# Kernel optimization log

Measured on AMD Instinct MI355X. Metric: run time of the kernel, lower is better.

## Reference

```python
import jax, jax.numpy as jnp
import numpy as np

U = 128            # channel (mode) size after split_mode
NUM_OUT_SEG = 16   # output segments


def setup_inputs() -> dict:
    key = jax.random.key(0)
    ks = jax.random.split(key, 16)
    B = 16384          # batch (num nodes)
    NUM_X0 = 10        # weight table rows (e.g. chemical elements)
    C = 300            # num_couplings (x0 segments)
    S = 32             # num_in_segments (x1 segments)
    P1, P2, P3 = 32, 64, 96  # paths per correlation degree 1,2,3
    inp = {
        'x0': jax.random.normal(ks[0], (NUM_X0, C * U), dtype=jnp.float32),
        'i0': jax.random.randint(ks[1], (B,), 0, NUM_X0),
        'x1': jax.random.normal(ks[2], (B, S * U), dtype=jnp.float32),
        'idx1': jax.random.randint(ks[3], (P1, 1), 0, S),
        'w1': jax.random.randint(ks[4], (P1,), 0, C),
        'o1': jax.random.randint(ks[5], (P1,), 0, NUM_OUT_SEG),
        'c1': jax.random.normal(ks[6], (P1,), dtype=jnp.float32),
        'idx2': jax.random.randint(ks[7], (P2, 2), 0, S),
        'w2': jax.random.randint(ks[8], (P2,), 0, C),
        'o2': jax.random.randint(ks[9], (P2,), 0, NUM_OUT_SEG),
        'c2': jax.random.normal(ks[10], (P2,), dtype=jnp.float32),
        'idx3': jax.random.randint(ks[11], (P3, 3), 0, S),
        'w3': jax.random.randint(ks[12], (P3,), 0, C),
        'o3': jax.random.randint(ks[13], (P3,), 0, NUM_OUT_SEG),
        'c3': jax.random.normal(ks[14], (P3,), dtype=jnp.float32),
    }
    return inp


def _symmetric_contraction(x0, i0, x1, paths):
    # x0: (num_x0, C*U) weight table, i0: (B,) gather index, x1: (B, S*U)
    B = x1.shape[0]
    g0 = x0.reshape(x0.shape[0], -1, U)[i0]   # (B, C, U) indexed gather
    x1r = x1.reshape(B, -1, U)                # (B, S, U)
    out = jnp.zeros((NUM_OUT_SEG, B, U), dtype=x1.dtype)
    for idx, w, o, c in paths:
        # path product: coeff * x0[i0][w_p] * prod_k x1[idx_{p,k}]
        t = g0[:, w] * c[None, :, None]       # (B, P, U)
        for k in range(idx.shape[1]):          # degree <= 3 (static)
            t = t * x1r[:, idx[:, k]]
        # scatter-add over output segments
        out = out + jax.ops.segment_sum(t.transpose(1, 0, 2), o,
                                        num_segments=NUM_OUT_SEG)
    return out.transpose(1, 0, 2).reshape(B, NUM_OUT_SEG * U)


def reference(x0, i0, x1, idx1, w1, o1, c1, idx2, w2, o2, c2,
              idx3, w3, o3, c3):
    paths = ((idx1, w1, o1, c1), (idx2, w2, o2, c2), (idx3, w3, o3, c3))
    return _symmetric_contraction(x0, i0, x1, paths)
```

## Files before the change

### kernel.cpp

```cpp
#include <hip/hip_runtime.h>
#include <hip/hip_bf16.h>

#define U_DIM 128
#define NUM_OUT_SEG 16
#define C_DIM 300
#define S_DIM 32
#define NUM_X0 10
#define P1 32
#define P2 64
#define P3 96
#define P_TOT (P1 + P2 + P3)

typedef float vfloat4 __attribute__((ext_vector_type(4)));

__global__ void prep_kernel(const int* __restrict__ idx1, const int* __restrict__ w1,
                            const int* __restrict__ o1, const float* __restrict__ c1,
                            const int* __restrict__ idx2, const int* __restrict__ w2,
                            const int* __restrict__ o2, const float* __restrict__ c2,
                            const int* __restrict__ idx3, const int* __restrict__ w3,
                            const int* __restrict__ o3, const float* __restrict__ c3,
                            int* __restrict__ soff, int2* __restrict__ meta) {
    __shared__ int cnt[48];
    __shared__ int off[49];
    __shared__ int cur[48];
    const int t = threadIdx.x;
    if (t < 48) cnt[t] = 0;
    __syncthreads();

    int key = -1, packed = 0;
    float c = 0.f;
    if (t < P_TOT) {
        int deg, o, w, a0 = 0, a1 = 0, a2 = 0;
        if (t < P1) {
            int p = t;
            deg = 1; w = w1[p]; o = o1[p]; c = c1[p];
            a0 = idx1[p];
        } else if (t < P1 + P2) {
            int p = t - P1;
            deg = 2; w = w2[p]; o = o2[p]; c = c2[p];
            a0 = idx2[2 * p]; a1 = idx2[2 * p + 1];
        } else {
            int p = t - P1 - P2;
            deg = 3; w = w3[p]; o = o3[p]; c = c3[p];
            a0 = idx3[3 * p]; a1 = idx3[3 * p + 1]; a2 = idx3[3 * p + 2];
        }
        key = o * 3 + (deg - 1);
        packed = w | (a0 << 9) | (a1 << 14) | (a2 << 19);
        atomicAdd(&cnt[key], 1);
    }
    __syncthreads();
    if (t == 0) {
        int a = 0;
        for (int k = 0; k < 48; ++k) { off[k] = a; a += cnt[k]; }
        off[48] = a;
    }
    __syncthreads();
    if (t < 49) soff[t] = off[t];
    if (t < 48) cur[t] = off[t];
    __syncthreads();
    if (t < P_TOT) {
        int r = atomicAdd(&cur[key], 1);
        meta[r] = make_int2(packed, __float_as_int(c));
    }
}

__global__ __launch_bounds__(1024, 8) void contract_kernel(
    const float* __restrict__ x0, const int* __restrict__ i0,
    const float* __restrict__ x1, const int* __restrict__ soff,
    const int2* __restrict__ gmeta, float* __restrict__ out) {
    __shared__ vfloat4 x1s[2 * S_DIM * 32];
    __shared__ int2 smeta[P_TOT];

    const int tid = threadIdx.x;
    const int wave = tid >> 6;
    const int lane = tid & 63;
    const int h = lane >> 5;
    const int ch = lane & 31;
    const long b0 = (long)blockIdx.x * 2;

    const vfloat4* x1p = (const vfloat4*)(x1 + b0 * (S_DIM * U_DIM));
    x1s[tid] = x1p[tid];
    x1s[tid + 1024] = x1p[tid + 1024];
    if (tid < P_TOT) smeta[tid] = gmeta[tid];

    const int elem = i0[b0 + h];
    const vfloat4* gseg = (const vfloat4*)x0 + (long)elem * (C_DIM * 32) + ch;
    const vfloat4* myx1 = x1s + h * (S_DIM * 32) + ch;

    int p = soff[wave * 3];
    const int e1 = soff[wave * 3 + 1];
    const int e2 = soff[wave * 3 + 2];
    const int e3 = soff[wave * 3 + 3];
    __syncthreads();

    vfloat4 acc = (vfloat4)(0.f);

#pragma unroll 2
    for (; p < e1; ++p) {
        int2 m = smeta[p];
        float cc = __int_as_float(m.y);
        vfloat4 g = gseg[(m.x & 0x1FF) * 32];
        vfloat4 xa = myx1[((m.x >> 9) & 31) * 32];
        acc += (cc * g) * xa;
    }
#pragma unroll 2
    for (; p < e2; ++p) {
        int2 m = smeta[p];
        float cc = __int_as_float(m.y);
        vfloat4 g = gseg[(m.x & 0x1FF) * 32];
        vfloat4 xa = myx1[((m.x >> 9) & 31) * 32];
        vfloat4 xb = myx1[((m.x >> 14) & 31) * 32];
        acc += (cc * g) * (xa * xb);
    }
#pragma unroll 2
    for (; p < e3; ++p) {
        int2 m = smeta[p];
        float cc = __int_as_float(m.y);
        vfloat4 g = gseg[(m.x & 0x1FF) * 32];
        vfloat4 xa = myx1[((m.x >> 9) & 31) * 32];
        vfloat4 xb = myx1[((m.x >> 14) & 31) * 32];
        vfloat4 xc = myx1[((m.x >> 19) & 31) * 32];
        acc += (cc * g) * (xa * xb * xc);
    }

    vfloat4* outp = (vfloat4*)(out + (b0 + h) * (NUM_OUT_SEG * U_DIM)) + wave * 32 + ch;
    __builtin_nontemporal_store(acc, outp);
}

extern "C" void kernel_launch(void* const* d_in, const int* in_sizes, int n_in,
                              void* d_out, int out_size, void* d_ws, size_t ws_size,
                              hipStream_t stream) {
    const float* x0 = (const float*)d_in[0];
    const int* i0 = (const int*)d_in[1];
    const float* x1 = (const float*)d_in[2];
    const int* idx1 = (const int*)d_in[3];
    const int* w1 = (const int*)d_in[4];
    const int* o1 = (const int*)d_in[5];
    const float* c1 = (const float*)d_in[6];
    const int* idx2 = (const int*)d_in[7];
    const int* w2 = (const int*)d_in[8];
    const int* o2 = (const int*)d_in[9];
    const float* c2 = (const float*)d_in[10];
    const int* idx3 = (const int*)d_in[11];
    const int* w3 = (const int*)d_in[12];
    const int* o3 = (const int*)d_in[13];
    const float* c3 = (const float*)d_in[14];

    int* soff = (int*)d_ws;
    int2* meta = (int2*)((char*)d_ws + 256);

    const int B = in_sizes[1];

    prep_kernel<<<1, 256, 0, stream>>>(idx1, w1, o1, c1, idx2, w2, o2, c2,
                                       idx3, w3, o3, c3, soff, meta);
    contract_kernel<<<B / 2, 1024, 0, stream>>>(x0, i0, x1, soff, meta, (float*)d_out);
}
```

Baseline: 439.7 us.

## Precompute coefficient-scaled x0 rows per path in a separate kernel

Adds a small kernel that, for each weight-table row and each sorted path, multiplies the x0 segment by the path coefficient and stores it contiguously in the workspace. The main kernel then reads the pre-scaled rows sequentially by path index, dropping a multiply and the coefficient load. The segment offsets are staged in shared memory, and each block rotates which output segment a wave handles to spread load. The extra launch and a small workspace table (10×192×128 floats) are added in exchange.

```diff
diff --git a/kernel.cpp b/kernel.cpp
--- a/kernel.cpp
+++ b/kernel.cpp
@@ -1,5 +1,4 @@
 #include <hip/hip_runtime.h>
-#include <hip/hip_bf16.h>
 
 #define U_DIM 128
 #define NUM_OUT_SEG 16
@@ -64,12 +63,27 @@
     }
 }
 
+__global__ __launch_bounds__(256) void scale_kernel(
+    const float* __restrict__ x0, const int2* __restrict__ meta,
+    vfloat4* __restrict__ g0c) {
+    const int idx = blockIdx.x * 256 + threadIdx.x;
+    const int u4 = idx & 31;
+    const int r = (idx >> 5) % P_TOT;
+    const int e = idx / (P_TOT * 32);
+    const int2 m = meta[r];
+    const int w = m.x & 0x1FF;
+    const float c = __int_as_float(m.y);
+    const vfloat4 v = ((const vfloat4*)x0)[((long)e * C_DIM + w) * 32 + u4];
+    g0c[idx] = c * v;
+}
+
 __global__ __launch_bounds__(1024, 8) void contract_kernel(
-    const float* __restrict__ x0, const int* __restrict__ i0,
+    const vfloat4* __restrict__ g0c, const int* __restrict__ i0,
     const float* __restrict__ x1, const int* __restrict__ soff,
     const int2* __restrict__ gmeta, float* __restrict__ out) {
     __shared__ vfloat4 x1s[2 * S_DIM * 32];
-    __shared__ int2 smeta[P_TOT];
+    __shared__ int smeta[P_TOT];
+    __shared__ int soffs[49];
 
     const int tid = threadIdx.x;
     const int wave = tid >> 6;
@@ -81,49 +95,49 @@
     const vfloat4* x1p = (const vfloat4*)(x1 + b0 * (S_DIM * U_DIM));
     x1s[tid] = x1p[tid];
     x1s[tid + 1024] = x1p[tid + 1024];
-    if (tid < P_TOT) smeta[tid] = gmeta[tid];
+    if (tid < P_TOT) smeta[tid] = gmeta[tid].x;
+    if (tid < 49) soffs[tid] = soff[tid];
 
     const int elem = i0[b0 + h];
-    const vfloat4* gseg = (const vfloat4*)x0 + (long)elem * (C_DIM * 32) + ch;
+    const vfloat4* gsegp = g0c + (long)elem * (P_TOT * 32) + ch;
     const vfloat4* myx1 = x1s + h * (S_DIM * 32) + ch;
 
-    int p = soff[wave * 3];
-    const int e1 = soff[wave * 3 + 1];
-    const int e2 = soff[wave * 3 + 2];
-    const int e3 = soff[wave * 3 + 3];
     __syncthreads();
+
+    const int sg = (wave + (int)blockIdx.x) & 15;
+    int p = soffs[sg * 3];
+    const int e1 = soffs[sg * 3 + 1];
+    const int e2 = soffs[sg * 3 + 2];
+    const int e3 = soffs[sg * 3 + 3];
 
     vfloat4 acc = (vfloat4)(0.f);
 
 #pragma unroll 2
     for (; p < e1; ++p) {
-        int2 m = smeta[p];
-        float cc = __int_as_float(m.y);
-        vfloat4 g = gseg[(m.x & 0x1FF) * 32];
-        vfloat4 xa = myx1[((m.x >> 9) & 31) * 32];
-        acc += (cc * g) * xa;
+        int mx = smeta[p];
+        vfloat4 g = gsegp[p * 32];
+        vfloat4 xa = myx1[((mx >> 9) & 31) * 32];
+        acc += g * xa;
     }
 #pragma unroll 2
     for (; p < e2; ++p) {
-        int2 m = smeta[p];
-        float cc = __int_as_float(m.y);
-        vfloat4 g = gseg[(m.x & 0x1FF) * 32];
-        vfloat4 xa = myx1[((m.x >> 9) & 31) * 32];
-        vfloat4 xb = myx1[((m.x >> 14) & 31) * 32];
-        acc += (cc * g) * (xa * xb);
+        int mx = smeta[p];
+        vfloat4 g = gsegp[p * 32];
+        vfloat4 xa = myx1[((mx >> 9) & 31) * 32];
+        vfloat4 xb = myx1[((mx >> 14) & 31) * 32];
+        acc += g * (xa * xb);
     }
-#pragma unroll 2
+#pragma unroll 4
     for (; p < e3; ++p) {
-        int2 m = smeta[p];
-        float cc = __int_as_float(m.y);
-        vfloat4 g = gseg[(m.x & 0x1FF) * 32];
-        vfloat4 xa = myx1[((m.x >> 9) & 31) * 32];
-        vfloat4 xb = myx1[((m.x >> 14) & 31) * 32];
-        vfloat4 xc = myx1[((m.x >> 19) & 31) * 32];
-        acc += (cc * g) * (xa * xb * xc);
+        int mx = smeta[p];
+        vfloat4 g = gsegp[p * 32];
+        vfloat4 xa = myx1[((mx >> 9) & 31) * 32];
+        vfloat4 xb = myx1[((mx >> 14) & 31) * 32];
+        vfloat4 xc = myx1[((mx >> 19) & 31) * 32];
+        acc += g * (xa * xb * xc);
     }
 
-    vfloat4* outp = (vfloat4*)(out + (b0 + h) * (NUM_OUT_SEG * U_DIM)) + wave * 32 + ch;
+    vfloat4* outp = (vfloat4*)(out + (b0 + h) * (NUM_OUT_SEG * U_DIM)) + sg * 32 + ch;
     __builtin_nontemporal_store(acc, outp);
 }
 
@@ -148,10 +162,12 @@
 
     int* soff = (int*)d_ws;
     int2* meta = (int2*)((char*)d_ws + 256);
+    vfloat4* g0c = (vfloat4*)((char*)d_ws + 4096);
 
     const int B = in_sizes[1];
 
     prep_kernel<<<1, 256, 0, stream>>>(idx1, w1, o1, c1, idx2, w2, o2, c2,
                                        idx3, w3, o3, c3, soff, meta);
-    contract_kernel<<<B / 2, 1024, 0, stream>>>(x0, i0, x1, soff, meta, (float*)d_out);
+    scale_kernel<<<(NUM_X0 * P_TOT * 32) / 256, 256, 0, stream>>>(x0, meta, g0c);
+    contract_kernel<<<B / 2, 1024, 0, stream>>>(g0c, i0, x1, soff, meta, (float*)d_out);
 }
```

Measured after the change: 448.0 us. No clear change (+1.9%).
